# Optimization experiments

Measured on AMD Instinct MI355X. Metric: run time of the kernel, lower is better.

Reference implementation:

```python
import jax, jax.numpy as jnp
import numpy as np

B, L = 1, 4096
VOCAB, D = 32000, 2048
NQ, NKV, HD = 16, 8, 128
EXPAND = NQ // NKV
SCALING = HD ** -0.5
SOFTCAP = 50.0
ROPE_THETA = 10000.0
RATIO = 0.25


def setup_inputs() -> dict:
    key = jax.random.key(0)
    k1, k2, k3, k4 = jax.random.split(key, 4)
    return {
        "input_ids": jax.random.randint(k1, (B, L), 0, VOCAB, dtype=jnp.int32),
        "embed_table": jax.random.normal(k2, (VOCAB, D), dtype=jnp.float32) * 0.02,
        "wq": jax.random.normal(k3, (D, NQ * HD), dtype=jnp.float32) * 0.02,
        "wk": jax.random.normal(k4, (D, NKV * HD), dtype=jnp.float32) * 0.02,
    }


def _rotate_half(x):
    h = x.shape[-1] // 2
    return jnp.concatenate([-x[..., h:], x[..., :h]], axis=-1)


def _importance(input_ids, embed_table, wq, wk):
    """QK + RoPE + softcap + causal softmax -> head/query-averaged importance [B, L]."""
    embs = embed_table[input_ids]  # [B, L, D]
    # rotary cos/sin: [1, 1, L, HD]
    inv_freq = 1.0 / (ROPE_THETA ** (jnp.arange(0, HD, 2, dtype=jnp.float32) / HD))
    freqs = jnp.arange(L, dtype=jnp.float32)[:, None] * inv_freq[None, :]  # [L, HD/2]
    emb = jnp.concatenate([freqs, freqs], axis=-1)
    cos = jnp.cos(emb)[None, None]
    sin = jnp.sin(emb)[None, None]
    q = (embs @ wq).reshape(B, L, NQ, HD).transpose(0, 2, 1, 3)   # [B, NQ, L, HD]
    k = (embs @ wk).reshape(B, L, NKV, HD).transpose(0, 2, 1, 3)  # [B, NKV, L, HD]
    q = q * cos + _rotate_half(q) * sin
    k = k * cos + _rotate_half(k) * sin
    k = jnp.repeat(k, EXPAND, axis=1)  # GQA expand -> [B, NQ, L, HD]
    scores = jnp.einsum('bhqd,bhkd->bhqk', q, k) * SCALING
    scores = jnp.tanh(scores / SOFTCAP) * SOFTCAP
    causal = jnp.triu(jnp.full((L, L), -jnp.inf, dtype=scores.dtype), 1)
    attn = jax.nn.softmax(scores + causal, axis=-1)  # [B, NQ, L, L]
    return attn.mean(axis=(1, 2))  # mean over heads then queries -> [B, L]


def reference(input_ids, embed_table, wq, wk):
    importance = _importance(input_ids, embed_table, wq, wk)
    k_sel = max(int(L * RATIO), 2)
    _, topk = jax.lax.top_k(importance, k_sel)
    topk = jnp.sort(topk, axis=-1)
    # Original torch code does `if need_append:` which requires B == 1.
    # Concrete (eager) branch; with random inputs this is almost always True.
    if bool(topk[0, -1] != L - 1):
        topk = jnp.concatenate([topk, jnp.full((B, 1), L - 1, dtype=topk.dtype)], axis=1)
    pruned_ids = jnp.take_along_axis(input_ids, topk, axis=1)
    return pruned_ids, topk
```

## Files before the change

### kernel.cpp

```cpp
#include <hip/hip_runtime.h>
#include <hip/hip_bf16.h>
#include <math.h>

#define L_SEQ   4096
#define D_MODEL 2048
#define NQ      16
#define NKV     8
#define HD      128
#define CSTR    3072
#define SCALING 0.08838834764831845f
#define LOG2E   1.4426950408889634f
#define K_SEL   1024
#define CHUNK   8
#define NCHUNK  288

typedef __attribute__((ext_vector_type(8))) short bf16x8;
typedef __attribute__((ext_vector_type(4))) float f32x4;

__device__ __forceinline__ unsigned short f2bf(float f) {
  union { float f; unsigned u; } v; v.f = f;
  unsigned r = v.u + 0x7fffu + ((v.u >> 16) & 1u);
  return (unsigned short)(r >> 16);
}
__device__ __forceinline__ unsigned pk2(float a, float b) {
  return (__float_as_uint(b) & 0xffff0000u) | (__float_as_uint(a) >> 16);
}
__device__ __forceinline__ float bf2f(unsigned short b) {
  union { unsigned u; float f; } v; v.u = ((unsigned)b) << 16;
  return v.f;
}

typedef __attribute__((address_space(3))) unsigned int lds_u32;
typedef const __attribute__((address_space(1))) unsigned int glob_u32;
__device__ __forceinline__ void gl2lds16(const unsigned short* g, unsigned short* l) {
  __builtin_amdgcn_global_load_lds((glob_u32*)g, (lds_u32*)l, 16, 0, 0);
}

#define PIPE_BARRIER_VM4()  do {                                   \
    asm volatile("s_waitcnt vmcnt(4)" ::: "memory");               \
    __builtin_amdgcn_sched_barrier(0);                             \
    __builtin_amdgcn_s_barrier();                                  \
    __builtin_amdgcn_sched_barrier(0);                             \
  } while (0)
#define PIPE_BARRIER_VM0()  do {                                   \
    asm volatile("s_waitcnt vmcnt(0)" ::: "memory");               \
    __builtin_amdgcn_sched_barrier(0);                             \
    __builtin_amdgcn_s_barrier();                                  \
    __builtin_amdgcn_sched_barrier(0);                             \
  } while (0)

__global__ __launch_bounds__(256) void prep_all(
    const int* __restrict__ ids, const float* __restrict__ table,
    const float* __restrict__ wq, const float* __restrict__ wk,
    unsigned short* __restrict__ A, unsigned short* __restrict__ Wt,
    float2* __restrict__ tab) {
  __shared__ __align__(16) unsigned short T[64][80];
  const int b = blockIdx.x;
  const int tid = threadIdx.x;
  if (b < 4096) {
    const float* src = table + (size_t)ids[b] * D_MODEL;
    const int c = tid * 8;
    const float4 f0 = *(const float4*)(src + c);
    const float4 f1 = *(const float4*)(src + c + 4);
    uint4 u;
    u.x = pk2(f0.x, f0.y); u.y = pk2(f0.z, f0.w);
    u.z = pk2(f1.x, f1.y); u.w = pk2(f1.z, f1.w);
    *(uint4*)(A + (size_t)b * D_MODEL + c) = u;
  } else if (b < 5632) {
    const int idx = b - 4096;
    const int nt = idx % 48;
    const int kt = idx / 48;
    const float* src; int srcN, n0;
    if (nt < 32) { src = wq; srcN = 2048; n0 = nt * 64; }
    else         { src = wk; srcN = 1024; n0 = (nt - 32) * 64; }
    const int k0 = kt * 64;
#pragma unroll
    for (int p = 0; p < 4; ++p) {
      const int i = p * 256 + tid;
      const int row = i >> 4;
      const int c4 = (i & 15) * 4;
      float4 v = *(const float4*)(src + (size_t)(k0 + row) * srcN + n0 + c4);
      T[c4 + 0][row] = f2bf(v.x); T[c4 + 1][row] = f2bf(v.y);
      T[c4 + 2][row] = f2bf(v.z); T[c4 + 3][row] = f2bf(v.w);
    }
    __syncthreads();
#pragma unroll
    for (int p = 0; p < 2; ++p) {
      const int c = p * 256 + tid;
      const int n = c >> 3, k8 = (c & 7) * 8;
      *(uint4*)(Wt + (size_t)(nt * 64 + n) * D_MODEL + k0 + k8) = *(const uint4*)(&T[n][k8]);
    }
  } else {
    const int g = (b - 5632) * 256 + tid;
    const int t = g & 63;
    const int i = g >> 6;
    const float invf = exp2f((float)t * (-13.287712379549449f / 64.0f));
    const float ang = (float)i * invf;
    tab[g] = make_float2(cosf(ang), sinf(ang));
  }
}

__global__ __launch_bounds__(256) void gemm_qk(
    const unsigned short* __restrict__ A,
    const unsigned short* __restrict__ Wt, unsigned short* __restrict__ C) {
  __shared__ __align__(16) unsigned short As[3][128 * 32];
  __shared__ __align__(16) unsigned short Bs[3][128 * 32];
  const int tid = threadIdx.x;
  const int w = tid >> 6, lane = tid & 63;
  const int quad = lane >> 4, lr = lane & 15;
  const int m0 = blockIdx.y * 128, n0 = blockIdx.x * 128;
  const int wm = (w >> 1) * 64, wn = (w & 1) * 64;

  const int srw = lane >> 2;
  const int schk = ((lane & 3) ^ ((lane >> 3) & 3)) * 8;
  const unsigned short* aptr0 = A + (size_t)(m0 + w * 16 + srw) * D_MODEL + schk;
  const unsigned short* aptr1 = aptr0 + (size_t)64 * D_MODEL;
  const unsigned short* bptr0 = Wt + (size_t)(n0 + w * 16 + srw) * D_MODEL + schk;
  const unsigned short* bptr1 = bptr0 + (size_t)64 * D_MODEL;
  const int sloff0 = (w * 16) * 32;
  const int sloff1 = (64 + w * 16) * 32;

  const int rsw = ((lr >> 1) & 3);

  f32x4 acc[4][4];
#pragma unroll
  for (int i = 0; i < 4; ++i)
#pragma unroll
    for (int j = 0; j < 4; ++j) acc[i][j] = (f32x4){0.f, 0.f, 0.f, 0.f};

  unsigned short *Aa = As[0], *Ab = As[1], *Ac = As[2];
  unsigned short *Ba = Bs[0], *Bb = Bs[1], *Bc = Bs[2];

  gl2lds16(aptr0, Aa + sloff0); gl2lds16(aptr1, Aa + sloff1);
  gl2lds16(bptr0, Ba + sloff0); gl2lds16(bptr1, Ba + sloff1);
  gl2lds16(aptr0 + 32, Ab + sloff0); gl2lds16(aptr1 + 32, Ab + sloff1);
  gl2lds16(bptr0 + 32, Bb + sloff0); gl2lds16(bptr1 + 32, Bb + sloff1);
  PIPE_BARRIER_VM4();

  for (int k0 = 0; k0 < D_MODEL; k0 += 32) {
    if (k0 + 64 < D_MODEL) {
      gl2lds16(aptr0 + k0 + 64, Ac + sloff0); gl2lds16(aptr1 + k0 + 64, Ac + sloff1);
      gl2lds16(bptr0 + k0 + 64, Bc + sloff0); gl2lds16(bptr1 + k0 + 64, Bc + sloff1);
    }
    bf16x8 af[4], bfr[4];
#pragma unroll
    for (int mt = 0; mt < 4; ++mt)
      af[mt] = *(const bf16x8*)&Aa[(wm + mt * 16 + lr) * 32 + (quad ^ rsw) * 8];
#pragma unroll
    for (int nt = 0; nt < 4; ++nt)
      bfr[nt] = *(const bf16x8*)&Ba[(wn + nt * 16 + lr) * 32 + (quad ^ rsw) * 8];
#pragma unroll
    for (int mt = 0; mt < 4; ++mt)
#pragma unroll
      for (int nt = 0; nt < 4; ++nt)
        acc[mt][nt] = __builtin_amdgcn_mfma_f32_16x16x32_bf16(af[mt], bfr[nt], acc[mt][nt], 0, 0, 0);
    if (k0 + 64 < D_MODEL) { PIPE_BARRIER_VM4(); } else { PIPE_BARRIER_VM0(); }
    unsigned short* t0 = Aa; Aa = Ab; Ab = Ac; Ac = t0;
    unsigned short* t1 = Ba; Ba = Bb; Bb = Bc; Bc = t1;
  }
#pragma unroll
  for (int mt = 0; mt < 4; ++mt) {
    const int row = m0 + wm + mt * 16 + quad * 4;
#pragma unroll
    for (int nt = 0; nt < 4; ++nt) {
      const int col = n0 + wn + nt * 16 + lr;
#pragma unroll
      for (int r = 0; r < 4; ++r)
        C[(size_t)(row + r) * CSTR + col] = f2bf(acc[mt][nt][r]);
    }
  }
}

__global__ __launch_bounds__(256) void rope_all(
    unsigned short* __restrict__ C, const float2* __restrict__ tab) {
  const int g = blockIdx.x * blockDim.x + threadIdx.x;
  const int t4 = (g & 15) * 4;
  const int hi = g >> 4;
  const int h = hi % 24;
  const int i = hi / 24;
  const size_t base = (size_t)i * CSTR + h * HD + t4;
  ushort4 a = *(const ushort4*)(C + base);
  ushort4 b = *(const ushort4*)(C + base + 64);
  const float2 cs0 = tab[i * 64 + t4 + 0];
  const float2 cs1 = tab[i * 64 + t4 + 1];
  const float2 cs2 = tab[i * 64 + t4 + 2];
  const float2 cs3 = tab[i * 64 + t4 + 3];
  const float a0 = bf2f(a.x), a1 = bf2f(a.y), a2 = bf2f(a.z), a3 = bf2f(a.w);
  const float b0 = bf2f(b.x), b1 = bf2f(b.y), b2 = bf2f(b.z), b3 = bf2f(b.w);
  ushort4 ra, rb;
  ra.x = f2bf(a0 * cs0.x - b0 * cs0.y); rb.x = f2bf(b0 * cs0.x + a0 * cs0.y);
  ra.y = f2bf(a1 * cs1.x - b1 * cs1.y); rb.y = f2bf(b1 * cs1.x + a1 * cs1.y);
  ra.z = f2bf(a2 * cs2.x - b2 * cs2.y); rb.z = f2bf(b2 * cs2.x + a2 * cs2.y);
  ra.w = f2bf(a3 * cs3.x - b3 * cs3.y); rb.w = f2bf(b3 * cs3.x + a3 * cs3.y);
  *(ushort4*)(C + base) = ra;
  *(ushort4*)(C + base + 64) = rb;
}

__device__ __forceinline__ void chunk_map(int bidx, int& bx, int& ch) {
  int rem = bidx;
  for (int b = 63; b >= 0; --b) {
    const int nc = (b + 2 + CHUNK - 1) >> 3;
    if (rem < nc) { bx = b; ch = rem; return; }
    rem -= nc;
  }
  bx = 0; ch = 0;
}

__device__ __forceinline__ void stage_k(
    const unsigned short* __restrict__ kb_lane,
    unsigned short* buf, int j0, int w) {
#pragma unroll
  for (int p = 0; p < 4; ++p)
    gl2lds16(kb_lane + (size_t)(j0 + p * 16) * CSTR, &buf[(p * 16 + w * 4) * 128]);
}

__global__ __launch_bounds__(256) void attn_z(
    const unsigned short* __restrict__ Qb,
    const unsigned short* __restrict__ Kb,
    float* __restrict__ Z) {
  __shared__ __align__(16) unsigned short Ks[3][64 * 128];
  const int tid = threadIdx.x;
  const int w = tid >> 6, lane = tid & 63;
  const int quad = lane >> 4, lr = lane & 15;
  const int kvh = blockIdx.y;
  int bx, ch; chunk_map(blockIdx.x, bx, ch);
  const int q0 = bx * 64;
  const int t0 = ch * CHUNK;
  const int t1 = min(t0 + CHUNK, bx + 1);

  const int srow = w * 4 + (lane >> 4);
  const int scol = (lane & 15) ^ (srow & 7);
  const unsigned short* kb_lane = Kb + (size_t)srow * CSTR + kvh * HD + scol * 8;

  int coff[4];
#pragma unroll
  for (int m = 0; m < 4; ++m) coff[m] = (((m * 4 + quad) ^ (lr & 7)) * 8);

  bf16x8 aq[2][4];
  const size_t rowb = (size_t)(q0 + w * 16 + lr) * CSTR;
#pragma unroll
  for (int hh = 0; hh < 2; ++hh)
#pragma unroll
    for (int m = 0; m < 4; ++m)
      aq[hh][m] = *(const bf16x8*)(Qb + rowb + (2 * kvh + hh) * HD + m * 32 + quad * 8);

  float zp[2][4] = {};

  unsigned short *pa = Ks[0], *pb = Ks[1], *pc = Ks[2];
  stage_k(kb_lane, pa, t0 * 64, w);
  if (t0 + 1 < t1) {
    stage_k(kb_lane, pb, (t0 + 1) * 64, w);
    PIPE_BARRIER_VM4();
  } else {
    PIPE_BARRIER_VM0();
  }
  for (int t = t0; t < t1; ++t) {
    if (t + 2 < t1) stage_k(kb_lane, pc, (t + 2) * 64, w);
    const unsigned short* kbuf = pa;
    const bool diag = (t == bx);
    const int nsub = diag ? (w + 1) : 4;
    for (int sub = 0; sub < nsub; ++sub) {
      bf16x8 bfr[4];
#pragma unroll
      for (int m = 0; m < 4; ++m)
        bfr[m] = *(const bf16x8*)&kbuf[(sub * 16 + lr) * 128 + coff[m]];
      const bool masked = diag && (sub == w);
#pragma unroll
      for (int hh = 0; hh < 2; ++hh) {
        f32x4 acc = {0.f, 0.f, 0.f, 0.f};
#pragma unroll
        for (int m = 0; m < 4; ++m)
          acc = __builtin_amdgcn_mfma_f32_16x16x32_bf16(aq[hh][m], bfr[m], acc, 0, 0, 0);
#pragma unroll
        for (int r = 0; r < 4; ++r) {
          float e = exp2f(acc[r] * (SCALING * LOG2E));
          if (masked && lr > quad * 4 + r) e = 0.0f;
          zp[hh][r] += e;
        }
      }
    }
    if (t + 2 < t1) { PIPE_BARRIER_VM4(); } else { PIPE_BARRIER_VM0(); }
    unsigned short* tmp = pa; pa = pb; pb = pc; pc = tmp;
  }
#pragma unroll
  for (int hh = 0; hh < 2; ++hh)
#pragma unroll
    for (int r = 0; r < 4; ++r) {
      float z = zp[hh][r];
      z += __shfl_xor(z, 1); z += __shfl_xor(z, 2);
      z += __shfl_xor(z, 4); z += __shfl_xor(z, 8);
      if (lr == 0)
        atomicAdd(&Z[(size_t)(2 * kvh + hh) * L_SEQ + q0 + w * 16 + quad * 4 + r], z);
    }
}

__global__ __launch_bounds__(256) void attn_col(
    const unsigned short* __restrict__ Qb,
    const unsigned short* __restrict__ Kb,
    const float* __restrict__ Z, float* __restrict__ imp) {
  __shared__ __align__(16) unsigned short Ks[3][64 * 128];
  __shared__ float colacc[CHUNK * 64];
  const int tid = threadIdx.x;
  const int w = tid >> 6, lane = tid & 63;
  const int quad = lane >> 4, lr = lane & 15;
  const int kvh = blockIdx.y;
  int bx, ch; chunk_map(blockIdx.x, bx, ch);
  const int q0 = bx * 64;
  const int t0 = ch * CHUNK;
  const int t1 = min(t0 + CHUNK, bx + 1);

  const int srow = w * 4 + (lane >> 4);
  const int scol = (lane & 15) ^ (srow & 7);
  const unsigned short* kb_lane = Kb + (size_t)srow * CSTR + kvh * HD + scol * 8;

  int coff[4];
#pragma unroll
  for (int m = 0; m < 4; ++m) coff[m] = (((m * 4 + quad) ^ (lr & 7)) * 8);

  bf16x8 aq[2][4];
  const size_t rowb = (size_t)(q0 + w * 16 + lr) * CSTR;
#pragma unroll
  for (int hh = 0; hh < 2; ++hh)
#pragma unroll
    for (int m = 0; m < 4; ++m)
      aq[hh][m] = *(const bf16x8*)(Qb + rowb + (2 * kvh + hh) * HD + m * 32 + quad * 8);

  float l2r[2][4];
#pragma unroll
  for (int hh = 0; hh < 2; ++hh) {
    const float4 z4 = *(const float4*)&Z[(size_t)(2 * kvh + hh) * L_SEQ + q0 + w * 16 + quad * 4];
    l2r[hh][0] = -__log2f(z4.x); l2r[hh][1] = -__log2f(z4.y);
    l2r[hh][2] = -__log2f(z4.z); l2r[hh][3] = -__log2f(z4.w);
  }

  for (int c = tid; c < CHUNK * 64; c += 256) colacc[c] = 0.0f;

  unsigned short *pa = Ks[0], *pb = Ks[1], *pc = Ks[2];
  stage_k(kb_lane, pa, t0 * 64, w);
  if (t0 + 1 < t1) {
    stage_k(kb_lane, pb, (t0 + 1) * 64, w);
    PIPE_BARRIER_VM4();
  } else {
    PIPE_BARRIER_VM0();
  }
  for (int t = t0; t < t1; ++t) {
    if (t + 2 < t1) stage_k(kb_lane, pc, (t + 2) * 64, w);
    const unsigned short* kbuf = pa;
    const bool diag = (t == bx);
    const int nsub = diag ? (w + 1) : 4;
    for (int sub = 0; sub < nsub; ++sub) {
      bf16x8 bfr[4];
#pragma unroll
      for (int m = 0; m < 4; ++m)
        bfr[m] = *(const bf16x8*)&kbuf[(sub * 16 + lr) * 128 + coff[m]];
      const bool masked = diag && (sub == w);
      float csum = 0.0f;
#pragma unroll
      for (int hh = 0; hh < 2; ++hh) {
        f32x4 acc = {0.f, 0.f, 0.f, 0.f};
#pragma unroll
        for (int m = 0; m < 4; ++m)
          acc = __builtin_amdgcn_mfma_f32_16x16x32_bf16(aq[hh][m], bfr[m], acc, 0, 0, 0);
#pragma unroll
        for (int r = 0; r < 4; ++r) {
          float e = exp2f(__builtin_fmaf(acc[r], SCALING * LOG2E, l2r[hh][r]));
          if (masked && lr > quad * 4 + r) e = 0.0f;
          csum += e;
        }
      }
      csum += __shfl_xor(csum, 16);
      csum += __shfl_xor(csum, 32);
      if (lane < 16) atomicAdd(&colacc[(t - t0) * 64 + sub * 16 + lr], csum);
    }
    if (t + 2 < t1) { PIPE_BARRIER_VM4(); } else { PIPE_BARRIER_VM0(); }
    unsigned short* tmp = pa; pa = pb; pb = pc; pc = tmp;
  }
  __syncthreads();
  const int ncol = (t1 - t0) * 64;
  const int jb = t0 * 64;
  for (int c = tid; c < ncol; c += 256) atomicAdd(&imp[jb + c], colacc[c]);
}

__global__ __launch_bounds__(1024) void topk_kernel(
    const float* __restrict__ imp, const int* __restrict__ ids,
    int* __restrict__ out, int out_size) {
  __shared__ unsigned vals[L_SEQ];
  __shared__ unsigned hist[256];
  __shared__ unsigned bc[2];
  __shared__ int wsum[16];
  __shared__ int wsum2[16];
  __shared__ int sel[K_SEL + 1];
  const int tid = threadIdx.x;
  const int lane = tid & 63, wv = tid >> 6;

  for (int i = tid; i < L_SEQ; i += 1024) vals[i] = __float_as_uint(imp[i]);
  __syncthreads();

  unsigned prefix = 0;
  int remaining = K_SEL;
#pragma unroll 1
  for (int shift = 24; shift >= 0; shift -= 8) {
    if (tid < 256) hist[tid] = 0;
    __syncthreads();
    const unsigned hmask = (shift == 24) ? 0u : (0xFFFFFFFFu << (shift + 8));
    for (int i = tid; i < L_SEQ; i += 1024) {
      const unsigned v = vals[i];
      if ((v & hmask) == prefix) atomicAdd(&hist[(v >> shift) & 255u], 1u);
    }
    __syncthreads();
    if (tid == 0) {
      unsigned cum = 0;
      for (int b = 255; b >= 0; --b) {
        const unsigned h = hist[b];
        if (cum + h >= (unsigned)remaining) { bc[0] = (unsigned)b; bc[1] = cum; break; }
        cum += h;
      }
    }
    __syncthreads();
    prefix |= bc[0] << shift;
    remaining -= (int)bc[1];
    __syncthreads();
  }
  const unsigned T = prefix;

  const int i0 = tid * 4;
  const unsigned v0 = vals[i0], v1 = vals[i0 + 1], v2 = vals[i0 + 2], v3 = vals[i0 + 3];
  const int e0 = (v0 == T), e1 = (v1 == T), e2 = (v2 == T), e3 = (v3 == T);
  const int eqc = e0 + e1 + e2 + e3;

  int x = eqc;
#pragma unroll
  for (int d = 1; d < 64; d <<= 1) { const int y = __shfl_up(x, d); if (lane >= d) x += y; }
  if (lane == 63) wsum[wv] = x;
  __syncthreads();
  if (tid < 16) {
    int s = wsum[tid];
#pragma unroll
    for (int d = 1; d < 16; d <<= 1) { const int y = __shfl_up(s, d); if (tid >= d) s += y; }
    wsum[tid] = s;
  }
  __syncthreads();
  const int eq_excl = (wv ? wsum[wv - 1] : 0) + x - eqc;
  const int r0 = eq_excl, r1 = r0 + e0, r2 = r1 + e1, r3 = r2 + e2;
  const int s0 = (v0 > T) || (e0 && r0 < remaining);
  const int s1 = (v1 > T) || (e1 && r1 < remaining);
  const int s2 = (v2 > T) || (e2 && r2 < remaining);
  const int s3 = (v3 > T) || (e3 && r3 < remaining);
  const int selc = s0 + s1 + s2 + s3;

  int x2 = selc;
#pragma unroll
  for (int d = 1; d < 64; d <<= 1) { const int y = __shfl_up(x2, d); if (lane >= d) x2 += y; }
  if (lane == 63) wsum2[wv] = x2;
  __syncthreads();
  if (tid < 16) {
    int s = wsum2[tid];
#pragma unroll
    for (int d = 1; d < 16; d <<= 1) { const int y = __shfl_up(s, d); if (tid >= d) s += y; }
    wsum2[tid] = s;
  }
  __syncthreads();
  int pos = (wv ? wsum2[wv - 1] : 0) + x2 - selc;
  if (s0) sel[pos++] = i0;
  if (s1) sel[pos++] = i0 + 1;
  if (s2) sel[pos++] = i0 + 2;
  if (s3) sel[pos++] = i0 + 3;
  if (tid == 0) sel[K_SEL] = L_SEQ - 1;
  __syncthreads();

  const int half = out_size >> 1;
  for (int i = tid; i < half; i += 1024) {
    const int idx2 = (i < K_SEL) ? sel[i] : sel[K_SEL];
    out[half + i] = idx2;
    out[i] = ids[idx2];
  }
}

extern "C" void kernel_launch(void* const* d_in, const int* in_sizes, int n_in,
                              void* d_out, int out_size, void* d_ws, size_t ws_size,
                              hipStream_t stream) {
  const int*   ids   = (const int*)d_in[0];
  const float* table = (const float*)d_in[1];
  const float* wq    = (const float*)d_in[2];
  const float* wk    = (const float*)d_in[3];
  char* ws = (char*)d_ws;
  unsigned short* Wt = (unsigned short*)ws;
  unsigned short* C  = (unsigned short*)(ws + 12ull * 1024 * 1024);
  float* imp = (float*)(ws + 36ull * 1024 * 1024);
  float* Z   = (float*)(ws + 36ull * 1024 * 1024 + 16384);
  float2* tab = (float2*)(ws + 38ull * 1024 * 1024);
  unsigned short* A = (unsigned short*)(ws + 40ull * 1024 * 1024);
  int* out = (int*)d_out;

  hipMemsetAsync(imp, 0, L_SEQ * sizeof(float), stream);
  hipMemsetAsync(Z, 0, NQ * L_SEQ * sizeof(float), stream);

  dim3 blk(256);
  prep_all<<<6656, blk, 0, stream>>>(ids, table, wq, wk, A, Wt, tab);
  gemm_qk<<<dim3(CSTR / 128, L_SEQ / 128), blk, 0, stream>>>(A, Wt, C);
  rope_all<<<(L_SEQ * 24 * 16) / 256, blk, 0, stream>>>(C, tab);
  attn_z<<<dim3(NCHUNK, NKV), blk, 0, stream>>>(C, C + 2048, Z);
  attn_col<<<dim3(NCHUNK, NKV), blk, 0, stream>>>(C, C + 2048, Z, imp);
  topk_kernel<<<1, 1024, 0, stream>>>(imp, ids, out, out_size);
}
```

Before: 591.5 us.

## Process 128 query rows per attention block to reuse staged K tiles

Both attention kernels (attn_z, attn_col) now cover two 64-row query sub-tiles per block. Each K tile staged into shared memory is used for both sub-tiles, which halves K loads per query row and halves the grid size. The chunk mapping is rewritten for 128-row blocks, and causal skipping is now decided per sub-tile. The triple-buffered K pipeline with explicit vmcnt barriers is replaced by a simpler double buffer with __syncthreads. This doubles the Q fragments held in registers and may weaken load/compute overlap.

Result: no change. 590.2 us (-0.2%).

```diff
diff --git a/kernel.cpp b/kernel.cpp
--- a/kernel.cpp
+++ b/kernel.cpp
@@ -12,7 +12,7 @@
 #define LOG2E   1.4426950408889634f
 #define K_SEL   1024
 #define CHUNK   8
-#define NCHUNK  288
+#define NCHUNK2 144
 
 typedef __attribute__((ext_vector_type(8))) short bf16x8;
 typedef __attribute__((ext_vector_type(4))) float f32x4;
@@ -119,7 +119,6 @@
   const unsigned short* bptr1 = bptr0 + (size_t)64 * D_MODEL;
   const int sloff0 = (w * 16) * 32;
   const int sloff1 = (64 + w * 16) * 32;
-
   const int rsw = ((lr >> 1) & 3);
 
   f32x4 acc[4][4];
@@ -196,10 +195,10 @@
   *(ushort4*)(C + base + 64) = rb;
 }
 
-__device__ __forceinline__ void chunk_map(int bidx, int& bx, int& ch) {
+__device__ __forceinline__ void chunk_map2(int bidx, int& bx, int& ch) {
   int rem = bidx;
-  for (int b = 63; b >= 0; --b) {
-    const int nc = (b + 2 + CHUNK - 1) >> 3;
+  for (int b = 31; b >= 0; --b) {
+    const int nc = (2 * b + 2 + CHUNK - 1) >> 3;
     if (rem < nc) { bx = b; ch = rem; return; }
     rem -= nc;
   }
@@ -218,15 +217,15 @@
     const unsigned short* __restrict__ Qb,
     const unsigned short* __restrict__ Kb,
     float* __restrict__ Z) {
-  __shared__ __align__(16) unsigned short Ks[3][64 * 128];
+  __shared__ __align__(16) unsigned short Ks[2][64 * 128];
   const int tid = threadIdx.x;
   const int w = tid >> 6, lane = tid & 63;
   const int quad = lane >> 4, lr = lane & 15;
   const int kvh = blockIdx.y;
-  int bx, ch; chunk_map(blockIdx.x, bx, ch);
-  const int q0 = bx * 64;
+  int bx, ch; chunk_map2(blockIdx.x, bx, ch);
+  const int q0 = bx * 128;
   const int t0 = ch * CHUNK;
-  const int t1 = min(t0 + CHUNK, bx + 1);
+  const int t1 = min(t0 + CHUNK, 2 * bx + 2);
 
   const int srow = w * 4 + (lane >> 4);
   const int scol = (lane & 15) ^ (srow & 7);
@@ -236,78 +235,81 @@
 #pragma unroll
   for (int m = 0; m < 4; ++m) coff[m] = (((m * 4 + quad) ^ (lr & 7)) * 8);
 
-  bf16x8 aq[2][4];
-  const size_t rowb = (size_t)(q0 + w * 16 + lr) * CSTR;
-#pragma unroll
-  for (int hh = 0; hh < 2; ++hh)
-#pragma unroll
-    for (int m = 0; m < 4; ++m)
-      aq[hh][m] = *(const bf16x8*)(Qb + rowb + (2 * kvh + hh) * HD + m * 32 + quad * 8);
-
-  float zp[2][4] = {};
-
-  unsigned short *pa = Ks[0], *pb = Ks[1], *pc = Ks[2];
-  stage_k(kb_lane, pa, t0 * 64, w);
-  if (t0 + 1 < t1) {
-    stage_k(kb_lane, pb, (t0 + 1) * 64, w);
-    PIPE_BARRIER_VM4();
-  } else {
-    PIPE_BARRIER_VM0();
-  }
+  bf16x8 aq[2][2][4];
+#pragma unroll
+  for (int s = 0; s < 2; ++s) {
+    const size_t rowb = (size_t)(q0 + s * 64 + w * 16 + lr) * CSTR;
+#pragma unroll
+    for (int hh = 0; hh < 2; ++hh)
+#pragma unroll
+      for (int m = 0; m < 4; ++m)
+        aq[s][hh][m] = *(const bf16x8*)(Qb + rowb + (2 * kvh + hh) * HD + m * 32 + quad * 8);
+  }
+
+  float zp[2][2][4] = {};
+
+  stage_k(kb_lane, Ks[0], t0 * 64, w);
+  __syncthreads();
+  int cur = 0;
   for (int t = t0; t < t1; ++t) {
-    if (t + 2 < t1) stage_k(kb_lane, pc, (t + 2) * 64, w);
-    const unsigned short* kbuf = pa;
-    const bool diag = (t == bx);
-    const int nsub = diag ? (w + 1) : 4;
-    for (int sub = 0; sub < nsub; ++sub) {
+    if (t + 1 < t1) stage_k(kb_lane, Ks[cur ^ 1], (t + 1) * 64, w);
+    const unsigned short* kbuf = Ks[cur];
+    for (int sub = 0; sub < 4; ++sub) {
       bf16x8 bfr[4];
 #pragma unroll
       for (int m = 0; m < 4; ++m)
         bfr[m] = *(const bf16x8*)&kbuf[(sub * 16 + lr) * 128 + coff[m]];
-      const bool masked = diag && (sub == w);
-#pragma unroll
-      for (int hh = 0; hh < 2; ++hh) {
-        f32x4 acc = {0.f, 0.f, 0.f, 0.f};
-#pragma unroll
-        for (int m = 0; m < 4; ++m)
-          acc = __builtin_amdgcn_mfma_f32_16x16x32_bf16(aq[hh][m], bfr[m], acc, 0, 0, 0);
-#pragma unroll
-        for (int r = 0; r < 4; ++r) {
-          float e = exp2f(acc[r] * (SCALING * LOG2E));
-          if (masked && lr > quad * 4 + r) e = 0.0f;
-          zp[hh][r] += e;
+#pragma unroll
+      for (int s = 0; s < 2; ++s) {
+        const int qt = 2 * bx + s;
+        if (t > qt || (t == qt && sub > w)) continue;
+        const bool masked = (t == qt) && (sub == w);
+#pragma unroll
+        for (int hh = 0; hh < 2; ++hh) {
+          f32x4 acc = {0.f, 0.f, 0.f, 0.f};
+#pragma unroll
+          for (int m = 0; m < 4; ++m)
+            acc = __builtin_amdgcn_mfma_f32_16x16x32_bf16(aq[s][hh][m], bfr[m], acc, 0, 0, 0);
+#pragma unroll
+          for (int r = 0; r < 4; ++r) {
+            float e = exp2f(acc[r] * (SCALING * LOG2E));
+            if (masked && lr > quad * 4 + r) e = 0.0f;
+            zp[s][hh][r] += e;
+          }
         }
       }
     }
-    if (t + 2 < t1) { PIPE_BARRIER_VM4(); } else { PIPE_BARRIER_VM0(); }
-    unsigned short* tmp = pa; pa = pb; pb = pc; pc = tmp;
-  }
-#pragma unroll
-  for (int hh = 0; hh < 2; ++hh)
-#pragma unroll
-    for (int r = 0; r < 4; ++r) {
-      float z = zp[hh][r];
-      z += __shfl_xor(z, 1); z += __shfl_xor(z, 2);
-      z += __shfl_xor(z, 4); z += __shfl_xor(z, 8);
-      if (lr == 0)
-        atomicAdd(&Z[(size_t)(2 * kvh + hh) * L_SEQ + q0 + w * 16 + quad * 4 + r], z);
-    }
+    __syncthreads();
+    cur ^= 1;
+  }
+#pragma unroll
+  for (int s = 0; s < 2; ++s)
+#pragma unroll
+    for (int hh = 0; hh < 2; ++hh)
+#pragma unroll
+      for (int r = 0; r < 4; ++r) {
+        float z = zp[s][hh][r];
+        z += __shfl_xor(z, 1); z += __shfl_xor(z, 2);
+        z += __shfl_xor(z, 4); z += __shfl_xor(z, 8);
+        if (lr == 0)
+          atomicAdd(&Z[(size_t)(2 * kvh + hh) * L_SEQ + q0 + s * 64 + w * 16 + quad * 4 + r], z);
+      }
 }
 
 __global__ __launch_bounds__(256) void attn_col(
     const unsigned short* __restrict__ Qb,
     const unsigned short* __restrict__ Kb,
     const float* __restrict__ Z, float* __restrict__ imp) {
-  __shared__ __align__(16) unsigned short Ks[3][64 * 128];
+  __shared__ __align__(16) unsigned short Ks[2][64 * 128];
   __shared__ float colacc[CHUNK * 64];
   const int tid = threadIdx.x;
   const int w = tid >> 6, lane = tid & 63;
   const int quad = lane >> 4, lr = lane & 15;
   const int kvh = blockIdx.y;
-  int bx, ch; chunk_map(blockIdx.x, bx, ch);
-  const int q0 = bx * 64;
+  int bx, ch; chunk_map2(blockIdx.x, bx, ch);
+  const int q0 = bx * 128;
   const int t0 = ch * CHUNK;
-  const int t1 = min(t0 + CHUNK, bx + 1);
+  const int t1 = min(t0 + CHUNK, 2 * bx + 2);
 
   const int srow = w * 4 + (lane >> 4);
   const int scol = (lane & 15) ^ (srow & 7);
@@ -317,65 +319,71 @@
 #pragma unroll
   for (int m = 0; m < 4; ++m) coff[m] = (((m * 4 + quad) ^ (lr & 7)) * 8);
 
-  bf16x8 aq[2][4];
-  const size_t rowb = (size_t)(q0 + w * 16 + lr) * CSTR;
-#pragma unroll
-  for (int hh = 0; hh < 2; ++hh)
-#pragma unroll
-    for (int m = 0; m < 4; ++m)
-      aq[hh][m] = *(const bf16x8*)(Qb + rowb + (2 * kvh + hh) * HD + m * 32 + quad * 8);
-
-  float l2r[2][4];
-#pragma unroll
-  for (int hh = 0; hh < 2; ++hh) {
-    const float4 z4 = *(const float4*)&Z[(size_t)(2 * kvh + hh) * L_SEQ + q0 + w * 16 + quad * 4];
-    l2r[hh][0] = -__log2f(z4.x); l2r[hh][1] = -__log2f(z4.y);
-    l2r[hh][2] = -__log2f(z4.z); l2r[hh][3] = -__log2f(z4.w);
-  }
+  bf16x8 aq[2][2][4];
+#pragma unroll
+  for (int s = 0; s < 2; ++s) {
+    const size_t rowb = (size_t)(q0 + s * 64 + w * 16 + lr) * CSTR;
+#pragma unroll
+    for (int hh = 0; hh < 2; ++hh)
+#pragma unroll
+      for (int m = 0; m < 4; ++m)
+        aq[s][hh][m] = *(const bf16x8*)(Qb + rowb + (2 * kvh + hh) * HD + m * 32 + quad * 8);
+  }
+
+  float l2r[2][2][4];
+#pragma unroll
+  for (int s = 0; s < 2; ++s)
+#pragma unroll
+    for (int hh = 0; hh < 2; ++hh) {
+      const float4 z4 = *(const float4*)&Z[(size_t)(2 * kvh + hh) * L_SEQ + q0 + s * 64 + w * 16 + quad * 4];
+      l2r[s][hh][0] = -__log2f(z4.x); l2r[s][hh][1] = -__log2f(z4.y);
+      l2r[s][hh][2] = -__log2f(z4.z); l2r[s][hh][3] = -__log2f(z4.w);
+    }
 
   for (int c = tid; c < CHUNK * 64; c += 256) colacc[c] = 0.0f;
 
-  unsigned short *pa = Ks[0], *pb = Ks[1], *pc = Ks[2];
-  stage_k(kb_lane, pa, t0 * 64, w);
-  if (t0 + 1 < t1) {
-    stage_k(kb_lane, pb, (t0 + 1) * 64, w);
-    PIPE_BARRIER_VM4();
-  } else {
-    PIPE_BARRIER_VM0();
-  }
+  stage_k(kb_lane, Ks[0], t0 * 64, w);
+  __syncthreads();
+  int cur = 0;
   for (int t = t0; t < t1; ++t) {
-    if (t + 2 < t1) stage_k(kb_lane, pc, (t + 2) * 64, w);
-    const unsigned short* kbuf = pa;
-    const bool diag = (t == bx);
-    const int nsub = diag ? (w + 1) : 4;
-    for (int sub = 0; sub < nsub; ++sub) {
+    if (t + 1 < t1) stage_k(kb_lane, Ks[cur ^ 1], (t + 1) * 64, w);
+    const unsigned short* kbuf = Ks[cur];
+    for (int sub = 0; sub < 4; ++sub) {
       bf16x8 bfr[4];
 #pragma unroll
       for (int m = 0; m < 4; ++m)
         bfr[m] = *(const bf16x8*)&kbuf[(sub * 16 + lr) * 128 + coff[m]];
-      const bool masked = diag && (sub == w);
       float csum = 0.0f;
-#pragma unroll
-      for (int hh = 0; hh < 2; ++hh) {
-        f32x4 acc = {0.f, 0.f, 0.f, 0.f};
-#pragma unroll
-        for (int m = 0; m < 4; ++m)
-          acc = __builtin_amdgcn_mfma_f32_16x16x32_bf16(aq[hh][m], bfr[m], acc, 0, 0, 0);
-#pragma unroll
-        for (int r = 0; r < 4; ++r) {
-          float e = exp2f(__builtin_fmaf(acc[r], SCALING * LOG2E, l2r[hh][r]));
-          if (masked && lr > quad * 4 + r) e = 0.0f;
-          csum += e;
+      bool any = false;
+#pragma unroll
+      for (int s = 0; s < 2; ++s) {
+        const int qt = 2 * bx + s;
+        if (t > qt || (t == qt && sub > w)) continue;
+        any = true;
+        const bool masked = (t == qt) && (sub == w);
+#pragma unroll
+        for (int hh = 0; hh < 2; ++hh) {
+          f32x4 acc = {0.f, 0.f, 0.f, 0.f};
+#pragma unroll
+          for (int m = 0; m < 4; ++m)
+            acc = __builtin_amdgcn_mfma_f32_16x16x32_bf16(aq[s][hh][m], bfr[m], acc, 0, 0, 0);
+#pragma unroll
+          for (int r = 0; r < 4; ++r) {
+            float e = exp2f(__builtin_fmaf(acc[r], SCALING * LOG2E, l2r[s][hh][r]));
+            if (masked && lr > quad * 4 + r) e = 0.0f;
+            csum += e;
+          }
         }
       }
-      csum += __shfl_xor(csum, 16);
-      csum += __shfl_xor(csum, 32);
-      if (lane < 16) atomicAdd(&colacc[(t - t0) * 64 + sub * 16 + lr], csum);
-    }
-    if (t + 2 < t1) { PIPE_BARRIER_VM4(); } else { PIPE_BARRIER_VM0(); }
-    unsigned short* tmp = pa; pa = pb; pb = pc; pc = tmp;
-  }
-  __syncthreads();
+      if (any) {
+        csum += __shfl_xor(csum, 16);
+        csum += __shfl_xor(csum, 32);
+        if (lane < 16) atomicAdd(&colacc[(t - t0) * 64 + sub * 16 + lr], csum);
+      }
+    }
+    __syncthreads();
+    cur ^= 1;
+  }
   const int ncol = (t1 - t0) * 64;
   const int jb = t0 * 64;
   for (int c = tid; c < ncol; c += 256) atomicAdd(&imp[jb + c], colacc[c]);
@@ -499,7 +507,7 @@
   prep_all<<<6656, blk, 0, stream>>>(ids, table, wq, wk, A, Wt, tab);
   gemm_qk<<<dim3(CSTR / 128, L_SEQ / 128), blk, 0, stream>>>(A, Wt, C);
   rope_all<<<(L_SEQ * 24 * 16) / 256, blk, 0, stream>>>(C, tab);
-  attn_z<<<dim3(NCHUNK, NKV), blk, 0, stream>>>(C, C + 2048, Z);
-  attn_col<<<dim3(NCHUNK, NKV), blk, 0, stream>>>(C, C + 2048, Z, imp);
+  attn_z<<<dim3(NCHUNK2, NKV), blk, 0, stream>>>(C, C + 2048, Z);
+  attn_col<<<dim3(NCHUNK2, NKV), blk, 0, stream>>>(C, C + 2048, Z, imp);
   topk_kernel<<<1, 1024, 0, stream>>>(imp, ids, out, out_size);
 }
```
